# Kernel optimization log

Measured on AMD Instinct MI355X. Metric: run time of the kernel, lower is better.

## Reference

```python
import jax, jax.numpy as jnp
import numpy as np

N_NODES = 50000
N_EDGES = 800000
IN_FEATS = 256
OUT_FEATS = 64
NUM_HEADS = 4
EDGE_FEATS = 64
NUM_ETYPES = 8
NEG_SLOPE = 0.2


def setup_inputs() -> dict:
    key = jax.random.key(0)
    ks = jax.random.split(key, 10)
    feat = jax.random.normal(ks[0], (N_NODES, IN_FEATS), dtype=jnp.float32)
    e_feat = jax.random.randint(ks[1], (N_EDGES,), 0, NUM_ETYPES)
    src = jax.random.randint(ks[2], (N_EDGES,), 0, N_NODES)
    dst = jax.random.randint(ks[3], (N_EDGES,), 0, N_NODES)
    # parameters (xavier-normal-ish scale)
    W_fc = jax.random.normal(ks[4], (IN_FEATS, NUM_HEADS * OUT_FEATS), dtype=jnp.float32) * 0.05
    W_e = jax.random.normal(ks[5], (EDGE_FEATS, NUM_HEADS * EDGE_FEATS), dtype=jnp.float32) * 0.1
    edge_emb = jax.random.normal(ks[6], (NUM_ETYPES, EDGE_FEATS), dtype=jnp.float32)
    attn_l = jax.random.normal(ks[7], (NUM_HEADS, OUT_FEATS), dtype=jnp.float32) * 0.1
    attn_r = jax.random.normal(ks[8], (NUM_HEADS, OUT_FEATS), dtype=jnp.float32) * 0.1
    attn_e = jax.random.normal(ks[9], (NUM_HEADS, EDGE_FEATS), dtype=jnp.float32) * 0.1
    return {"feat": feat, "e_feat": e_feat, "src": src, "dst": dst,
            "W_fc": W_fc, "W_e": W_e, "edge_emb": edge_emb,
            "attn_l": attn_l, "attn_r": attn_r, "attn_e": attn_e}


def reference(feat, e_feat, src, dst, W_fc, W_e, edge_emb, attn_l, attn_r, attn_e):
    N = feat.shape[0]
    H, D = attn_l.shape
    # node projection: [N, H, D]
    ft = (feat @ W_fc).reshape(N, H, D)
    # edge-type embedding -> per-head edge feature: [E, H, edge_feats]
    ef = (edge_emb[e_feat] @ W_e).reshape(-1, H, attn_e.shape[1])
    ee = jnp.einsum('ehf,hf->eh', ef, attn_e)          # [E, H]
    el = jnp.einsum('nhd,hd->nh', ft, attn_l)          # [N, H]
    er = jnp.einsum('nhd,hd->nh', ft, attn_r)          # [N, H]
    # edge logits: u_add_v + edge-type term, leaky relu
    e = el[src] + er[dst] + ee                          # [E, H]
    e = jnp.where(e > 0, e, NEG_SLOPE * e)
    # segment softmax grouped by destination node
    m = jax.ops.segment_max(e, dst, num_segments=N)     # [N, H]
    ex = jnp.exp(e - m[dst])
    s = jax.ops.segment_sum(ex, dst, num_segments=N)    # [N, H]
    a = ex / s[dst]                                     # [E, H]
    # weighted scatter-sum aggregation: sum_e ft[src_e] * a_e -> dst_e
    rst = jax.ops.segment_sum(ft[src] * a[:, :, None], dst, num_segments=N)  # [N, H, D]
    return rst, a
```

## Files before the change

### kernel.cpp

```cpp
#include <hip/hip_runtime.h>

#define H 4
#define D 64
#define C 256
#define IN_F 256
#define EF 64
#define NEG 0.2f

typedef unsigned short ushort_t;
typedef __attribute__((ext_vector_type(8))) short bf16x8;
typedef __attribute__((ext_vector_type(4))) float f32x4;

__device__ __forceinline__ ushort_t f2bf(float x) {
    unsigned u = __float_as_uint(x);
    unsigned r = u + 0x7FFFu + ((u >> 16) & 1u);
    return (ushort_t)(r >> 16);
}

__global__ void k_etype(const float* __restrict__ edge_emb, const float* __restrict__ W_e,
                        const float* __restrict__ attn_e, float* __restrict__ ee) {
    int t = blockIdx.x;
    int c = threadIdx.x;
    float acc = 0.f;
    #pragma unroll 8
    for (int k = 0; k < EF; ++k)
        acc += edge_emb[t * EF + k] * W_e[k * C + c];
    acc *= attn_e[c];
    #pragma unroll
    for (int s = 32; s > 0; s >>= 1) acc += __shfl_down(acc, s, 64);
    if ((threadIdx.x & 63) == 0) ee[t * H + (threadIdx.x >> 6)] = acc;
}

__global__ void k_wt(const float* __restrict__ W, ushort_t* __restrict__ WT) {
    int n = blockIdx.x, k = threadIdx.x;
    WT[n * 256 + k] = f2bf(W[(size_t)k * 256 + n]);
}

#define BM 128
#define BN 128
#define BK 64
__launch_bounds__(256, 2)
__global__ void k_gemm(const float* __restrict__ feat, const ushort_t* __restrict__ Bbf,
                       const float* __restrict__ attn_l, const float* __restrict__ attn_r,
                       ushort_t* __restrict__ ftbf, float* __restrict__ el, float* __restrict__ er,
                       int N) {
    __shared__ ushort_t As[BM * BK];
    __shared__ ushort_t Bs[BN * BK];
    int t = threadIdx.x;
    int l = t & 63, w = t >> 6;
    int wr = w >> 1, wc = w & 1;
    int m0 = blockIdx.x * BM;
    int n0 = blockIdx.y * BN;

    f32x4 zero = {0.f, 0.f, 0.f, 0.f};
    f32x4 acc[4][4];
    #pragma unroll
    for (int i = 0; i < 4; ++i)
        #pragma unroll
        for (int j = 0; j < 4; ++j) acc[i][j] = zero;

    for (int ks = 0; ks < 4; ++ks) {
        #pragma unroll
        for (int i = 0; i < 4; ++i) {
            int c   = t + i * 256;
            int row = c >> 3;
            int kg  = c & 7;
            int kgs = kg ^ (row & 7);
            int gr = m0 + row;
            float4 a0 = {0.f,0.f,0.f,0.f}, a1 = {0.f,0.f,0.f,0.f};
            if (gr < N) {
                const float* ap = feat + (size_t)gr * 256 + ks * BK + kg * 8;
                a0 = *(const float4*)ap;
                a1 = *(const float4*)(ap + 4);
            }
            ushort_t v[8];
            v[0]=f2bf(a0.x); v[1]=f2bf(a0.y); v[2]=f2bf(a0.z); v[3]=f2bf(a0.w);
            v[4]=f2bf(a1.x); v[5]=f2bf(a1.y); v[6]=f2bf(a1.z); v[7]=f2bf(a1.w);
            *(uint4*)(&As[row * BK + kgs * 8]) = *(uint4*)v;
            *(uint4*)(&Bs[row * BK + kgs * 8]) =
                *(const uint4*)(Bbf + (size_t)(n0 + row) * 256 + ks * BK + kg * 8);
        }
        __syncthreads();
        #pragma unroll
        for (int k2 = 0; k2 < 2; ++k2) {
            bf16x8 av[4], bv[4];
            int kc = (l >> 4) + k2 * 4;
            #pragma unroll
            for (int i = 0; i < 4; ++i) {
                int ra = wr * 64 + i * 16 + (l & 15);
                av[i] = *(const bf16x8*)(&As[ra * BK + (kc ^ (ra & 7)) * 8]);
                int rb = wc * 64 + i * 16 + (l & 15);
                bv[i] = *(const bf16x8*)(&Bs[rb * BK + (kc ^ (rb & 7)) * 8]);
            }
            #pragma unroll
            for (int i = 0; i < 4; ++i)
                #pragma unroll
                for (int j = 0; j < 4; ++j)
                    acc[i][j] = __builtin_amdgcn_mfma_f32_16x16x32_bf16(av[i], bv[j], acc[i][j], 0, 0, 0);
        }
        __syncthreads();
    }

    int cb = n0 + wc * 64;
    int h  = cb >> 6;
    float wl[4], wrg[4];
    #pragma unroll
    for (int j = 0; j < 4; ++j) {
        int d = j * 16 + (l & 15);
        wl[j]  = attn_l[h * 64 + d];
        wrg[j] = attn_r[h * 64 + d];
    }
    int rbase = m0 + wr * 64;
    #pragma unroll
    for (int i = 0; i < 4; ++i) {
        #pragma unroll
        for (int r = 0; r < 4; ++r) {
            int m = rbase + i * 16 + (l >> 4) * 4 + r;
            float pl = 0.f, pr = 0.f;
            #pragma unroll
            for (int j = 0; j < 4; ++j) {
                float v = acc[i][j][r];
                ftbf[(size_t)m * 256 + cb + j * 16 + (l & 15)] = f2bf(v);
                pl = fmaf(v, wl[j], pl);
                pr = fmaf(v, wrg[j], pr);
            }
            #pragma unroll
            for (int s2 = 1; s2 <= 8; s2 <<= 1) {
                pl += __shfl_xor(pl, s2, 64);
                pr += __shfl_xor(pr, s2, 64);
            }
            if ((l & 15) == 0 && m < N) { el[m * H + h] = pl; er[m * H + h] = pr; }
        }
    }
}

__global__ void k_deg(const int* __restrict__ dst, unsigned* __restrict__ deg, int E) {
    int i = (blockIdx.x * 256 + threadIdx.x) * 4;
    if (i + 3 < E) {
        int4 d = *(const int4*)(dst + i);
        atomicAdd(&deg[d.x], 1u); atomicAdd(&deg[d.y], 1u);
        atomicAdd(&deg[d.z], 1u); atomicAdd(&deg[d.w], 1u);
    } else {
        for (int k = 0; k < 4; ++k)
            if (i + k < E) atomicAdd(&deg[dst[i + k]], 1u);
    }
}

__global__ void k_scan(const unsigned* __restrict__ deg, unsigned* __restrict__ off, int n) {
    __shared__ unsigned wsum[16];
    __shared__ unsigned carry_s;
    int t = threadIdx.x;
    int lane = t & 63, wv = t >> 6;
    if (t == 0) carry_s = 0;
    __syncthreads();
    int ns = n + 1;
    int ntile = (ns + 4095) >> 12;
    for (int tile = 0; tile < ntile; ++tile) {
        int i0 = (tile << 12) + t * 4;
        uint4 v;
        if (i0 + 3 < n) {
            v = *(const uint4*)(deg + i0);
        } else {
            v.x = (i0 + 0 < n) ? deg[i0 + 0] : 0u;
            v.y = (i0 + 1 < n) ? deg[i0 + 1] : 0u;
            v.z = (i0 + 2 < n) ? deg[i0 + 2] : 0u;
            v.w = (i0 + 3 < n) ? deg[i0 + 3] : 0u;
        }
        unsigned s = v.x + v.y + v.z + v.w;
        unsigned sc = s;
        #pragma unroll
        for (int d = 1; d < 64; d <<= 1) {
            unsigned u = __shfl_up(sc, d, 64);
            if (lane >= d) sc += u;
        }
        if (lane == 63) wsum[wv] = sc;
        __syncthreads();
        unsigned carry = carry_s;
        unsigned woff = 0;
        #pragma unroll
        for (int k = 0; k < 16; ++k) woff += (k < wv) ? wsum[k] : 0u;
        unsigned ex0 = carry + woff + sc - s;
        uint4 o;
        o.x = ex0; o.y = ex0 + v.x; o.z = o.y + v.y; o.w = o.z + v.z;
        *(uint4*)(off + i0) = o;
        __syncthreads();
        if (t == 1023) carry_s = carry + woff + sc;
    }
}

__global__ void k_scatlog(const int* __restrict__ dst, const int* __restrict__ src,
                          const int* __restrict__ efeat, const unsigned* __restrict__ off,
                          unsigned* __restrict__ cursor,
                          const float4* __restrict__ el4, const float4* __restrict__ er4,
                          const float4* __restrict__ ee4,
                          float4* __restrict__ exq, uint2* __restrict__ es, int E) {
    int e = blockIdx.x * 256 + threadIdx.x;
    if (e >= E) return;
    int d = dst[e], s = src[e];
    unsigned q = off[d] + atomicAdd(&cursor[d], 1u);
    float4 l = el4[s];
    float4 r = er4[d];
    float4 te = ee4[efeat[e]];
    float4 v;
    v.x = l.x + r.x + te.x; v.y = l.y + r.y + te.y;
    v.z = l.z + r.z + te.z; v.w = l.w + r.w + te.w;
    v.x = v.x > 0.f ? v.x : NEG * v.x;
    v.y = v.y > 0.f ? v.y : NEG * v.y;
    v.z = v.z > 0.f ? v.z : NEG * v.z;
    v.w = v.w > 0.f ? v.w : NEG * v.w;
    v.x = __expf(v.x); v.y = __expf(v.y); v.z = __expf(v.z); v.w = __expf(v.w);
    exq[q] = v;
    es[q] = make_uint2((unsigned)e, (unsigned)s);
}

__device__ __forceinline__ void macc8(float* acc, uint4 f, float a) {
    unsigned u[4] = {f.x, f.y, f.z, f.w};
    #pragma unroll
    for (int q = 0; q < 4; ++q) {
        float lo = __uint_as_float(u[q] << 16);
        float hi = __uint_as_float(u[q] & 0xFFFF0000u);
        acc[2*q]   = fmaf(lo, a, acc[2*q]);
        acc[2*q+1] = fmaf(hi, a, acc[2*q+1]);
    }
}

__launch_bounds__(256)
__global__ void k_agg(const unsigned* __restrict__ off, const uint2* __restrict__ es,
                      const float* __restrict__ exs, const ushort_t* __restrict__ ft,
                      float4* __restrict__ out4, float* __restrict__ out_a, int N) {
    int node = (int)((blockIdx.x * (size_t)blockDim.x + threadIdx.x) >> 6);
    if (node >= N) return;
    int lane = threadIdx.x & 63;
    unsigned beg = off[node], end = off[node + 1];

    int h1 = lane >> 4, i16 = lane & 15;
    float s = 0.f;
    for (unsigned j = beg + i16; j < end; j += 16)
        s += exs[j * 4 + h1];
    #pragma unroll
    for (int m = 1; m <= 8; m <<= 1) s += __shfl_xor(s, m, 64);
    float inv_h = (end > beg) ? 1.f / s : 0.f;

    int half = lane >> 5;
    int cl   = lane & 31;
    int h2   = cl >> 3;
    float inv2 = __shfl(inv_h, h2 * 16, 64);
    float inva = __shfl(inv_h, (lane & 3) * 16, 64);

    float acc[8];
    #pragma unroll
    for (int q = 0; q < 8; ++q) acc[q] = 0.f;

    unsigned j = beg;
    uint2 cur;
    if (j + half < end) cur = es[j + half];
    for (; j + 1 < end; j += 2) {
        unsigned jj = j + half;
        uint2 e2 = cur;
        float a  = exs[jj * 4 + h2] * inv2;
        float aw = exs[jj * 4 + (lane & 3)];
        unsigned jn = jj + 2;
        if (jn < end) cur = es[jn];
        uint4 f = *(const uint4*)(ft + (size_t)e2.y * 256 + cl * 8);
        macc8(acc, f, a);
        if (cl < 4) out_a[e2.x * 4 + cl] = aw * inva;
    }
    if (j < end) {
        uint2 e2 = es[j];
        float a = (half == 0) ? exs[j * 4 + h2] * inv2 : 0.f;
        uint4 f = *(const uint4*)(ft + (size_t)e2.y * 256 + cl * 8);
        macc8(acc, f, a);
        if (lane < 4) out_a[e2.x * 4 + lane] = exs[j * 4 + lane] * inva;
    }

    #pragma unroll
    for (int q = 0; q < 8; ++q) acc[q] += __shfl_xor(acc[q], 32, 64);
    if (half == 0) {
        float4 o0 = {acc[0], acc[1], acc[2], acc[3]};
        float4 o1 = {acc[4], acc[5], acc[6], acc[7]};
        out4[(size_t)node * 64 + cl * 2]     = o0;
        out4[(size_t)node * 64 + cl * 2 + 1] = o1;
    }
}

extern "C" void kernel_launch(void* const* d_in, const int* in_sizes, int n_in,
                              void* d_out, int out_size, void* d_ws, size_t ws_size,
                              hipStream_t stream) {
    const float* feat     = (const float*)d_in[0];
    const int*   e_feat   = (const int*)d_in[1];
    const int*   src      = (const int*)d_in[2];
    const int*   dst      = (const int*)d_in[3];
    const float* W_fc     = (const float*)d_in[4];
    const float* W_e      = (const float*)d_in[5];
    const float* edge_emb = (const float*)d_in[6];
    const float* attn_l   = (const float*)d_in[7];
    const float* attn_r   = (const float*)d_in[8];
    const float* attn_e   = (const float*)d_in[9];

    int N = in_sizes[0] / IN_F;
    int E = in_sizes[1];
    int Mpad = ((N + BM - 1) / BM) * BM;
    int Npad4  = (N + 3) & ~3;
    int offpad = (((N + 1) + 4095) >> 12) << 12;
    int Epad2  = (E + 1) & ~1;

    float* out_rst = (float*)d_out;
    float* out_a   = out_rst + (size_t)N * C;

    ushort_t* WTbf = (ushort_t*)d_ws;
    ushort_t* ftbf = WTbf + 256 * 256;
    float* el = (float*)(ftbf + (size_t)Mpad * 256);
    float* er = el + (size_t)N * H;
    float* ee = er + (size_t)N * H;
    unsigned* deg    = (unsigned*)(ee + 64);
    unsigned* off    = deg + Npad4;
    unsigned* cursor = off + offpad;
    uint2*    es     = (uint2*)(cursor + Npad4);
    float4*   exq    = (float4*)(es + Epad2);

    hipMemsetAsync(deg, 0, (size_t)Npad4 * sizeof(unsigned), stream);
    hipMemsetAsync(cursor, 0, (size_t)Npad4 * sizeof(unsigned), stream);

    k_etype  <<<8, 256, 0, stream>>>(edge_emb, W_e, attn_e, ee);
    k_wt     <<<256, 256, 0, stream>>>(W_fc, WTbf);
    {
        dim3 grid(Mpad / BM, C / BN);
        k_gemm <<<grid, 256, 0, stream>>>(feat, WTbf, attn_l, attn_r, ftbf, el, er, N);
    }
    k_deg    <<<(E / 4 + 255) / 256, 256, 0, stream>>>(dst, deg, E);
    k_scan   <<<1, 1024, 0, stream>>>(deg, off, N);
    k_scatlog<<<(E + 255) / 256, 256, 0, stream>>>(dst, src, e_feat, off, cursor,
                                                   (const float4*)el, (const float4*)er,
                                                   (const float4*)ee, exq, es, E);
    k_agg    <<<((size_t)N * 64 + 255) / 256, 256, 0, stream>>>(off, es, (const float*)exq,
                                                                ftbf, (float4*)out_rst, out_a, N);
}
```

Baseline: 328.6 us.

## Fuse prep kernels, widen GEMM tile to full width, restructure aggregation

```diff
diff --git a/kernel.cpp b/kernel.cpp
--- a/kernel.cpp
+++ b/kernel.cpp
@@ -17,40 +17,52 @@
     return (ushort_t)(r >> 16);
 }
 
-__global__ void k_etype(const float* __restrict__ edge_emb, const float* __restrict__ W_e,
-                        const float* __restrict__ attn_e, float* __restrict__ ee) {
-    int t = blockIdx.x;
-    int c = threadIdx.x;
-    float acc = 0.f;
-    #pragma unroll 8
-    for (int k = 0; k < EF; ++k)
-        acc += edge_emb[t * EF + k] * W_e[k * C + c];
-    acc *= attn_e[c];
-    #pragma unroll
-    for (int s = 32; s > 0; s >>= 1) acc += __shfl_down(acc, s, 64);
-    if ((threadIdx.x & 63) == 0) ee[t * H + (threadIdx.x >> 6)] = acc;
-}
-
-__global__ void k_wt(const float* __restrict__ W, ushort_t* __restrict__ WT) {
-    int n = blockIdx.x, k = threadIdx.x;
-    WT[n * 256 + k] = f2bf(W[(size_t)k * 256 + n]);
+__global__ void k_misc(const float* __restrict__ W, ushort_t* __restrict__ WT,
+                       const float* __restrict__ edge_emb, const float* __restrict__ W_e,
+                       const float* __restrict__ attn_e, float* __restrict__ ee) {
+    int b = blockIdx.x;
+    if (b < 16) {
+        __shared__ float tile[64][65];
+        int bi = b >> 2, bj = b & 3;
+        int lane = threadIdx.x & 63, wv = threadIdx.x >> 6;
+        #pragma unroll
+        for (int i = 0; i < 16; ++i) {
+            int row = wv * 16 + i;
+            tile[row][lane] = W[(size_t)(bi * 64 + row) * 256 + bj * 64 + lane];
+        }
+        __syncthreads();
+        #pragma unroll
+        for (int i = 0; i < 16; ++i) {
+            int row = wv * 16 + i;
+            WT[(size_t)(bj * 64 + row) * 256 + bi * 64 + lane] = f2bf(tile[lane][row]);
+        }
+    } else {
+        int t = b - 16;
+        int c = threadIdx.x;
+        float acc = 0.f;
+        #pragma unroll 8
+        for (int k = 0; k < EF; ++k)
+            acc += edge_emb[t * EF + k] * W_e[k * C + c];
+        acc *= attn_e[c];
+        #pragma unroll
+        for (int s = 32; s > 0; s >>= 1) acc += __shfl_down(acc, s, 64);
+        if ((threadIdx.x & 63) == 0) ee[t * H + (threadIdx.x >> 6)] = acc;
+    }
 }
 
 #define BM 128
-#define BN 128
 #define BK 64
-__launch_bounds__(256, 2)
+__launch_bounds__(512)
 __global__ void k_gemm(const float* __restrict__ feat, const ushort_t* __restrict__ Bbf,
                        const float* __restrict__ attn_l, const float* __restrict__ attn_r,
                        ushort_t* __restrict__ ftbf, float* __restrict__ el, float* __restrict__ er,
                        int N) {
     __shared__ ushort_t As[BM * BK];
-    __shared__ ushort_t Bs[BN * BK];
+    __shared__ ushort_t Bs[C * BK];
     int t = threadIdx.x;
     int l = t & 63, w = t >> 6;
-    int wr = w >> 1, wc = w & 1;
+    int wr = w >> 2, wc = w & 3;
     int m0 = blockIdx.x * BM;
-    int n0 = blockIdx.y * BN;
 
     f32x4 zero = {0.f, 0.f, 0.f, 0.f};
     f32x4 acc[4][4];
@@ -61,8 +73,8 @@
 
     for (int ks = 0; ks < 4; ++ks) {
         #pragma unroll
-        for (int i = 0; i < 4; ++i) {
-            int c   = t + i * 256;
+        for (int i = 0; i < 2; ++i) {
+            int c   = t + i * 512;
             int row = c >> 3;
             int kg  = c & 7;
             int kgs = kg ^ (row & 7);
@@ -77,8 +89,15 @@
             v[0]=f2bf(a0.x); v[1]=f2bf(a0.y); v[2]=f2bf(a0.z); v[3]=f2bf(a0.w);
             v[4]=f2bf(a1.x); v[5]=f2bf(a1.y); v[6]=f2bf(a1.z); v[7]=f2bf(a1.w);
             *(uint4*)(&As[row * BK + kgs * 8]) = *(uint4*)v;
+        }
+        #pragma unroll
+        for (int i = 0; i < 4; ++i) {
+            int c   = t + i * 512;
+            int row = c >> 3;
+            int kg  = c & 7;
+            int kgs = kg ^ (row & 7);
             *(uint4*)(&Bs[row * BK + kgs * 8]) =
-                *(const uint4*)(Bbf + (size_t)(n0 + row) * 256 + ks * BK + kg * 8);
+                *(const uint4*)(Bbf + (size_t)row * 256 + ks * BK + kg * 8);
         }
         __syncthreads();
         #pragma unroll
@@ -101,8 +120,8 @@
         __syncthreads();
     }
 
-    int cb = n0 + wc * 64;
-    int h  = cb >> 6;
+    int cb = wc * 64;
+    int h  = wc;
     float wl[4], wrg[4];
     #pragma unroll
     for (int j = 0; j < 4; ++j) {
@@ -146,7 +165,8 @@
     }
 }
 
-__global__ void k_scan(const unsigned* __restrict__ deg, unsigned* __restrict__ off, int n) {
+__global__ void k_scan(const unsigned* __restrict__ deg, unsigned* __restrict__ off,
+                       unsigned* __restrict__ cursor, int n) {
     __shared__ unsigned wsum[16];
     __shared__ unsigned carry_s;
     int t = threadIdx.x;
@@ -183,13 +203,14 @@
         uint4 o;
         o.x = ex0; o.y = ex0 + v.x; o.z = o.y + v.y; o.w = o.z + v.z;
         *(uint4*)(off + i0) = o;
+        *(uint4*)(cursor + i0) = o;
         __syncthreads();
         if (t == 1023) carry_s = carry + woff + sc;
     }
 }
 
 __global__ void k_scatlog(const int* __restrict__ dst, const int* __restrict__ src,
-                          const int* __restrict__ efeat, const unsigned* __restrict__ off,
+                          const int* __restrict__ efeat,
                           unsigned* __restrict__ cursor,
                           const float4* __restrict__ el4, const float4* __restrict__ er4,
                           const float4* __restrict__ ee4,
@@ -197,7 +218,7 @@
     int e = blockIdx.x * 256 + threadIdx.x;
     if (e >= E) return;
     int d = dst[e], s = src[e];
-    unsigned q = off[d] + atomicAdd(&cursor[d], 1u);
+    unsigned q = atomicAdd(&cursor[d], 1u);
     float4 l = el4[s];
     float4 r = er4[d];
     float4 te = ee4[efeat[e]];
@@ -241,45 +262,54 @@
     for (int m = 1; m <= 8; m <<= 1) s += __shfl_xor(s, m, 64);
     float inv_h = (end > beg) ? 1.f / s : 0.f;
 
-    int half = lane >> 5;
-    int cl   = lane & 31;
-    int h2   = cl >> 3;
+    int g  = lane >> 4;
+    int li = lane & 15;
+    int h2 = li >> 2;
     float inv2 = __shfl(inv_h, h2 * 16, 64);
     float inva = __shfl(inv_h, (lane & 3) * 16, 64);
 
-    float acc[8];
-    #pragma unroll
-    for (int q = 0; q < 8; ++q) acc[q] = 0.f;
+    float acc[16];
+    #pragma unroll
+    for (int q = 0; q < 16; ++q) acc[q] = 0.f;
 
     unsigned j = beg;
-    uint2 cur;
-    if (j + half < end) cur = es[j + half];
-    for (; j + 1 < end; j += 2) {
-        unsigned jj = j + half;
-        uint2 e2 = cur;
+    for (; j + 3 < end; j += 4) {
+        unsigned jj = j + g;
+        uint2 e2 = es[jj];
         float a  = exs[jj * 4 + h2] * inv2;
         float aw = exs[jj * 4 + (lane & 3)];
-        unsigned jn = jj + 2;
-        if (jn < end) cur = es[jn];
-        uint4 f = *(const uint4*)(ft + (size_t)e2.y * 256 + cl * 8);
-        macc8(acc, f, a);
-        if (cl < 4) out_a[e2.x * 4 + cl] = aw * inva;
+        const ushort_t* fp = ft + (size_t)e2.y * 256 + li * 16;
+        uint4 f0 = *(const uint4*)fp;
+        uint4 f1 = *(const uint4*)(fp + 8);
+        macc8(acc, f0, a);
+        macc8(acc + 8, f1, a);
+        if (li < 4) out_a[e2.x * 4 + li] = aw * inva;
     }
     if (j < end) {
-        uint2 e2 = es[j];
-        float a = (half == 0) ? exs[j * 4 + h2] * inv2 : 0.f;
-        uint4 f = *(const uint4*)(ft + (size_t)e2.y * 256 + cl * 8);
-        macc8(acc, f, a);
-        if (lane < 4) out_a[e2.x * 4 + lane] = exs[j * 4 + lane] * inva;
-    }
-
-    #pragma unroll
-    for (int q = 0; q < 8; ++q) acc[q] += __shfl_xor(acc[q], 32, 64);
-    if (half == 0) {
-        float4 o0 = {acc[0], acc[1], acc[2], acc[3]};
-        float4 o1 = {acc[4], acc[5], acc[6], acc[7]};
-        out4[(size_t)node * 64 + cl * 2]     = o0;
-        out4[(size_t)node * 64 + cl * 2 + 1] = o1;
+        unsigned jj = j + g;
+        bool act = jj < end;
+        unsigned jc = act ? jj : beg;
+        uint2 e2 = es[jc];
+        float a = act ? exs[jc * 4 + h2] * inv2 : 0.f;
+        const ushort_t* fp = ft + (size_t)e2.y * 256 + li * 16;
+        uint4 f0 = *(const uint4*)fp;
+        uint4 f1 = *(const uint4*)(fp + 8);
+        macc8(acc, f0, a);
+        macc8(acc + 8, f1, a);
+        if (act && li < 4) out_a[e2.x * 4 + li] = exs[jc * 4 + li] * inva;
+    }
+
+    #pragma unroll
+    for (int q = 0; q < 16; ++q) {
+        acc[q] += __shfl_xor(acc[q], 16, 64);
+        acc[q] += __shfl_xor(acc[q], 32, 64);
+    }
+    if (g == 0) {
+        #pragma unroll
+        for (int k = 0; k < 4; ++k) {
+            float4 o = {acc[k*4], acc[k*4+1], acc[k*4+2], acc[k*4+3]};
+            out4[(size_t)node * 64 + li * 4 + k] = o;
+        }
     }
 }
 
@@ -299,8 +329,7 @@
 
     int N = in_sizes[0] / IN_F;
     int E = in_sizes[1];
-    int Mpad = ((N + BM - 1) / BM) * BM;
-    int Npad4  = (N + 3) & ~3;
+    int Mpad   = ((N + BM - 1) / BM) * BM;
     int offpad = (((N + 1) + 4095) >> 12) << 12;
     int Epad2  = (E + 1) & ~1;
 
@@ -313,23 +342,18 @@
     float* er = el + (size_t)N * H;
     float* ee = er + (size_t)N * H;
     unsigned* deg    = (unsigned*)(ee + 64);
-    unsigned* off    = deg + Npad4;
+    unsigned* off    = deg + offpad;
     unsigned* cursor = off + offpad;
-    uint2*    es     = (uint2*)(cursor + Npad4);
+    uint2*    es     = (uint2*)(cursor + offpad);
     float4*   exq    = (float4*)(es + Epad2);
 
-    hipMemsetAsync(deg, 0, (size_t)Npad4 * sizeof(unsigned), stream);
-    hipMemsetAsync(cursor, 0, (size_t)Npad4 * sizeof(unsigned), stream);
-
-    k_etype  <<<8, 256, 0, stream>>>(edge_emb, W_e, attn_e, ee);
-    k_wt     <<<256, 256, 0, stream>>>(W_fc, WTbf);
-    {
-        dim3 grid(Mpad / BM, C / BN);
-        k_gemm <<<grid, 256, 0, stream>>>(feat, WTbf, attn_l, attn_r, ftbf, el, er, N);
-    }
+    hipMemsetAsync(deg, 0, (size_t)offpad * sizeof(unsigned), stream);
+
+    k_misc   <<<24, 256, 0, stream>>>(W_fc, WTbf, edge_emb, W_e, attn_e, ee);
     k_deg    <<<(E / 4 + 255) / 256, 256, 0, stream>>>(dst, deg, E);
-    k_scan   <<<1, 1024, 0, stream>>>(deg, off, N);
-    k_scatlog<<<(E + 255) / 256, 256, 0, stream>>>(dst, src, e_feat, off, cursor,
+    k_scan   <<<1, 1024, 0, stream>>>(deg, off, cursor, N);
+    k_gemm   <<<Mpad / BM, 512, 0, stream>>>(feat, WTbf, attn_l, attn_r, ftbf, el, er, N);
+    k_scatlog<<<(E + 255) / 256, 256, 0, stream>>>(dst, src, e_feat, cursor,
                                                    (const float4*)el, (const float4*)er,
                                                    (const float4*)ee, exq, es, E);
     k_agg    <<<((size_t)N * 64 + 255) / 256, 256, 0, stream>>>(off, es, (const float*)exq,
```

Result: faster. 309.8 us (-5.7%).
